# Optimization experiments

Hardware: AMD Instinct MI355X
Metric: run time of the kernel (lower is better)

Reference implementation:

```python
import jax, jax.numpy as jnp
import numpy as np

TAU = 1.0


def setup_inputs() -> dict:
    key = jax.random.key(0)
    k1, k2 = jax.random.split(key)
    z = jax.random.normal(k1, (131072, 64), dtype=jnp.float32)
    cluster_centers = jax.random.normal(k2, (512, 64), dtype=jnp.float32)
    return {"z": z, "cluster_centers": cluster_centers}


def reference(z, cluster_centers):
    # ||z - c||^2 = ||z||^2 + ||c||^2 - 2 z.c  (avoids the [B,K,D] broadcast tensor)
    z_sq = jnp.sum(z * z, axis=1, keepdims=True)              # [B, 1]
    c_sq = jnp.sum(cluster_centers * cluster_centers, axis=1)  # [K]
    cross = jnp.einsum('bd,kd->bk', z, cluster_centers)        # [B, K]
    dist_sq = z_sq + c_sq[None, :] - 2.0 * cross               # [B, K]
    q = jax.nn.softmax(-dist_sq / TAU, axis=1)                 # [B, K]
    loss = jnp.mean(jnp.sum(q * dist_sq, axis=1))
    return (q, loss)
```

## Files before the change

kernel.cpp:

```cpp
#include <hip/hip_runtime.h>

typedef short bf16x8 __attribute__((ext_vector_type(8)));
typedef float f32x4 __attribute__((ext_vector_type(4)));

#define K_CLUSTERS 512
#define DIM 64
#define ROWS_PER_BLOCK 64

__device__ __forceinline__ unsigned short f32_to_bf16_rne(float f) {
    unsigned int u = __float_as_uint(f);
    u += 0x7fffu + ((u >> 16) & 1u);
    return (unsigned short)(u >> 16);
}
__device__ __forceinline__ float bf16_bits_to_f32(unsigned short h) {
    return __uint_as_float(((unsigned int)h) << 16);
}

__global__ void prep_centers(const float* __restrict__ c,
                             short* __restrict__ c_hi, short* __restrict__ c_lo,
                             float* __restrict__ c_sq) {
    int idx = blockIdx.x * 256 + threadIdx.x;
    float v = c[idx];
    unsigned short h = f32_to_bf16_rne(v);
    float hf = bf16_bits_to_f32(h);
    unsigned short l = f32_to_bf16_rne(v - hf);
    c_hi[idx] = (short)h;
    c_lo[idx] = (short)l;
    float s = v * v;
    #pragma unroll
    for (int off = 1; off < 64; off <<= 1) s += __shfl_xor(s, off, 64);
    if ((threadIdx.x & 63) == 0) c_sq[idx >> 6] = s;
}

__global__ void init_loss(float* __restrict__ loss_out) {
    if (threadIdx.x == 0) loss_out[0] = 0.0f;
}

__global__ __launch_bounds__(256, 2)
void cluster_kernel(const float* __restrict__ z,
                    const short* __restrict__ c_hi,
                    const short* __restrict__ c_lo,
                    const float* __restrict__ c_sq,
                    float* __restrict__ q_out,
                    float* __restrict__ loss_out,
                    float inv_b) {
    __shared__ __align__(16) short a_hi_s[16][72];
    __shared__ __align__(16) short a_lo_s[16][72];
    __shared__ float zsq_s[16];
    __shared__ float dist_s[16][K_CLUSTERS + 4];
    __shared__ float wloss_s[4];

    const int tid  = threadIdx.x;
    const int lane = tid & 63;
    const int wave = tid >> 6;
    const int m    = lane & 15;
    const int qd   = lane >> 4;
    const long rb  = (long)blockIdx.x * ROWS_PER_BLOCK;

    bf16x8 bh[8][2], bl[8][2];
    float csq[8];
    #pragma unroll
    for (int t = 0; t < 8; ++t) {
        const int col = wave * 128 + t * 16 + m;
        const long boff = (long)col * DIM + qd * 8;
        #pragma unroll
        for (int kg = 0; kg < 2; ++kg) {
            bh[t][kg] = *(const bf16x8*)(c_hi + boff + kg * 32);
            bl[t][kg] = *(const bf16x8*)(c_lo + boff + kg * 32);
        }
        csq[t] = c_sq[col];
    }

    float4 v = ((const float4*)(z + rb * DIM))[tid];
    float lsum = 0.0f;

    for (int s = 0; s < ROWS_PER_BLOCK / 16; ++s) {
        float4 vn;
        if (s + 1 < ROWS_PER_BLOCK / 16)
            vn = ((const float4*)(z + (rb + (s + 1) * 16) * DIM))[tid];

        {
            const int srow = tid >> 4;
            const int scol = (tid & 15) * 4;
            float fv[4] = {v.x, v.y, v.z, v.w};
            #pragma unroll
            for (int j = 0; j < 4; ++j) {
                unsigned short h = f32_to_bf16_rne(fv[j]);
                float hf = bf16_bits_to_f32(h);
                unsigned short l = f32_to_bf16_rne(fv[j] - hf);
                a_hi_s[srow][scol + j] = (short)h;
                a_lo_s[srow][scol + j] = (short)l;
            }
            float ssq = fv[0]*fv[0] + fv[1]*fv[1] + fv[2]*fv[2] + fv[3]*fv[3];
            #pragma unroll
            for (int off = 1; off < 16; off <<= 1) ssq += __shfl_xor(ssq, off, 64);
            if ((tid & 15) == 0) zsq_s[srow] = ssq;
        }
        __syncthreads();

        bf16x8 ah[2], al[2];
        #pragma unroll
        for (int kg = 0; kg < 2; ++kg) {
            ah[kg] = *(const bf16x8*)&a_hi_s[m][kg * 32 + qd * 8];
            al[kg] = *(const bf16x8*)&a_lo_s[m][kg * 32 + qd * 8];
        }

        f32x4 acc[8];
        #pragma unroll
        for (int t = 0; t < 8; ++t) acc[t] = (f32x4){0.f, 0.f, 0.f, 0.f};
        #pragma unroll
        for (int kg = 0; kg < 2; ++kg) {
            #pragma unroll
            for (int t = 0; t < 8; ++t) {
                acc[t] = __builtin_amdgcn_mfma_f32_16x16x32_bf16(ah[kg], bh[t][kg], acc[t], 0, 0, 0);
                acc[t] = __builtin_amdgcn_mfma_f32_16x16x32_bf16(ah[kg], bl[t][kg], acc[t], 0, 0, 0);
                acc[t] = __builtin_amdgcn_mfma_f32_16x16x32_bf16(al[kg], bh[t][kg], acc[t], 0, 0, 0);
            }
        }

        #pragma unroll
        for (int t = 0; t < 8; ++t) {
            const int col = wave * 128 + t * 16 + m;
            #pragma unroll
            for (int r = 0; r < 4; ++r) {
                const int row = qd * 4 + r;
                dist_s[row][col] = zsq_s[row] + csq[t] - 2.0f * acc[t][r];
            }
        }
        __syncthreads();

        const long rbase = rb + s * 16;
        #pragma unroll
        for (int rr = 0; rr < 4; ++rr) {
            const int row = wave * 4 + rr;
            float d[8];
            #pragma unroll
            for (int j = 0; j < 8; ++j) d[j] = dist_s[row][lane + 64 * j];
            float mn = d[0];
            #pragma unroll
            for (int j = 1; j < 8; ++j) mn = fminf(mn, d[j]);
            #pragma unroll
            for (int off = 1; off < 64; off <<= 1) mn = fminf(mn, __shfl_xor(mn, off, 64));
            float e[8], ssum = 0.0f;
            #pragma unroll
            for (int j = 0; j < 8; ++j) { e[j] = __expf(mn - d[j]); ssum += e[j]; }
            #pragma unroll
            for (int off = 1; off < 64; off <<= 1) ssum += __shfl_xor(ssum, off, 64);
            const float inv = 1.0f / ssum;
            float rl = 0.0f;
            float* orow = q_out + (rbase + row) * K_CLUSTERS;
            #pragma unroll
            for (int j = 0; j < 8; ++j) {
                const float qv = e[j] * inv;
                orow[lane + 64 * j] = qv;
                rl += qv * d[j];
            }
            #pragma unroll
            for (int off = 1; off < 64; off <<= 1) rl += __shfl_xor(rl, off, 64);
            lsum += rl;
        }
        v = vn;
    }

    if (lane == 0) wloss_s[wave] = lsum;
    __syncthreads();
    if (tid == 0)
        atomicAdd(loss_out, (wloss_s[0] + wloss_s[1] + wloss_s[2] + wloss_s[3]) * inv_b);
}

extern "C" void kernel_launch(void* const* d_in, const int* in_sizes, int n_in,
                              void* d_out, int out_size, void* d_ws, size_t ws_size,
                              hipStream_t stream) {
    const float* z = (const float*)d_in[0];
    const float* c = (const float*)d_in[1];
    const int B = in_sizes[0] / DIM;
    float* q_out = (float*)d_out;
    float* loss_out = q_out + (size_t)B * K_CLUSTERS;

    char* ws = (char*)d_ws;
    short* c_hi = (short*)ws;
    short* c_lo = (short*)(ws + 65536);
    float* c_sq = (float*)(ws + 131072);

    prep_centers<<<(K_CLUSTERS * DIM) / 256, 256, 0, stream>>>(c, c_hi, c_lo, c_sq);
    init_loss<<<1, 64, 0, stream>>>(loss_out);
    cluster_kernel<<<B / ROWS_PER_BLOCK, 256, 0, stream>>>(z, c_hi, c_lo, c_sq, q_out,
                                                           loss_out, 1.0f / (float)B);
}
```

Baseline: 343.1 us.

## Split work across 8 waves per block and use nontemporal q stores

Doubles the block to 512 threads so each wave holds centroid fragments for 64 clusters instead of 128 and handles 2 softmax rows instead of 4. This cuts register pressure and raises occupancy. It also writes q with nontemporal stores, moves the loss shuffle reduction out of the row loop, and folds the loss zeroing into prep_centers to drop one launch. The cost is more redundant z staging per block and more barrier participants.

```diff
diff --git a/kernel.cpp b/kernel.cpp
--- a/kernel.cpp
+++ b/kernel.cpp
@@ -18,7 +18,8 @@
 
 __global__ void prep_centers(const float* __restrict__ c,
                              short* __restrict__ c_hi, short* __restrict__ c_lo,
-                             float* __restrict__ c_sq) {
+                             float* __restrict__ c_sq, float* __restrict__ loss_out) {
+    if (blockIdx.x == 0 && threadIdx.x == 0) loss_out[0] = 0.0f;
     int idx = blockIdx.x * 256 + threadIdx.x;
     float v = c[idx];
     unsigned short h = f32_to_bf16_rne(v);
@@ -32,11 +33,7 @@
     if ((threadIdx.x & 63) == 0) c_sq[idx >> 6] = s;
 }
 
-__global__ void init_loss(float* __restrict__ loss_out) {
-    if (threadIdx.x == 0) loss_out[0] = 0.0f;
-}
-
-__global__ __launch_bounds__(256, 2)
+__global__ __launch_bounds__(512, 4)
 void cluster_kernel(const float* __restrict__ z,
                     const short* __restrict__ c_hi,
                     const short* __restrict__ c_lo,
@@ -48,7 +45,7 @@
     __shared__ __align__(16) short a_lo_s[16][72];
     __shared__ float zsq_s[16];
     __shared__ float dist_s[16][K_CLUSTERS + 4];
-    __shared__ float wloss_s[4];
+    __shared__ float wloss_s[8];
 
     const int tid  = threadIdx.x;
     const int lane = tid & 63;
@@ -57,11 +54,11 @@
     const int qd   = lane >> 4;
     const long rb  = (long)blockIdx.x * ROWS_PER_BLOCK;
 
-    bf16x8 bh[8][2], bl[8][2];
-    float csq[8];
+    bf16x8 bh[4][2], bl[4][2];
+    float csq[4];
     #pragma unroll
-    for (int t = 0; t < 8; ++t) {
-        const int col = wave * 128 + t * 16 + m;
+    for (int t = 0; t < 4; ++t) {
+        const int col = wave * 64 + t * 16 + m;
         const long boff = (long)col * DIM + qd * 8;
         #pragma unroll
         for (int kg = 0; kg < 2; ++kg) {
@@ -71,30 +68,30 @@
         csq[t] = c_sq[col];
     }
 
-    float4 v = ((const float4*)(z + rb * DIM))[tid];
+    const float2* zin = (const float2*)(z + rb * DIM);
+    float2 v = zin[tid];
     float lsum = 0.0f;
 
     for (int s = 0; s < ROWS_PER_BLOCK / 16; ++s) {
-        float4 vn;
-        if (s + 1 < ROWS_PER_BLOCK / 16)
-            vn = ((const float4*)(z + (rb + (s + 1) * 16) * DIM))[tid];
+        float2 vn;
+        if (s + 1 < ROWS_PER_BLOCK / 16) vn = zin[(s + 1) * 512 + tid];
 
         {
-            const int srow = tid >> 4;
-            const int scol = (tid & 15) * 4;
-            float fv[4] = {v.x, v.y, v.z, v.w};
+            const int srow = tid >> 5;
+            const int scol = (tid & 31) * 2;
+            float fv[2] = {v.x, v.y};
             #pragma unroll
-            for (int j = 0; j < 4; ++j) {
+            for (int j = 0; j < 2; ++j) {
                 unsigned short h = f32_to_bf16_rne(fv[j]);
                 float hf = bf16_bits_to_f32(h);
                 unsigned short l = f32_to_bf16_rne(fv[j] - hf);
                 a_hi_s[srow][scol + j] = (short)h;
                 a_lo_s[srow][scol + j] = (short)l;
             }
-            float ssq = fv[0]*fv[0] + fv[1]*fv[1] + fv[2]*fv[2] + fv[3]*fv[3];
+            float ssq = fv[0] * fv[0] + fv[1] * fv[1];
             #pragma unroll
-            for (int off = 1; off < 16; off <<= 1) ssq += __shfl_xor(ssq, off, 64);
-            if ((tid & 15) == 0) zsq_s[srow] = ssq;
+            for (int off = 1; off < 32; off <<= 1) ssq += __shfl_xor(ssq, off, 64);
+            if ((tid & 31) == 0) zsq_s[srow] = ssq;
         }
         __syncthreads();
 
@@ -105,13 +102,13 @@
             al[kg] = *(const bf16x8*)&a_lo_s[m][kg * 32 + qd * 8];
         }
 
-        f32x4 acc[8];
+        f32x4 acc[4];
         #pragma unroll
-        for (int t = 0; t < 8; ++t) acc[t] = (f32x4){0.f, 0.f, 0.f, 0.f};
+        for (int t = 0; t < 4; ++t) acc[t] = (f32x4){0.f, 0.f, 0.f, 0.f};
         #pragma unroll
         for (int kg = 0; kg < 2; ++kg) {
             #pragma unroll
-            for (int t = 0; t < 8; ++t) {
+            for (int t = 0; t < 4; ++t) {
                 acc[t] = __builtin_amdgcn_mfma_f32_16x16x32_bf16(ah[kg], bh[t][kg], acc[t], 0, 0, 0);
                 acc[t] = __builtin_amdgcn_mfma_f32_16x16x32_bf16(ah[kg], bl[t][kg], acc[t], 0, 0, 0);
                 acc[t] = __builtin_amdgcn_mfma_f32_16x16x32_bf16(al[kg], bh[t][kg], acc[t], 0, 0, 0);
@@ -119,8 +116,8 @@
         }
 
         #pragma unroll
-        for (int t = 0; t < 8; ++t) {
-            const int col = wave * 128 + t * 16 + m;
+        for (int t = 0; t < 4; ++t) {
+            const int col = wave * 64 + t * 16 + m;
             #pragma unroll
             for (int r = 0; r < 4; ++r) {
                 const int row = qd * 4 + r;
@@ -131,8 +128,8 @@
 
         const long rbase = rb + s * 16;
         #pragma unroll
-        for (int rr = 0; rr < 4; ++rr) {
-            const int row = wave * 4 + rr;
+        for (int rr = 0; rr < 2; ++rr) {
+            const int row = wave * 2 + rr;
             float d[8];
             #pragma unroll
             for (int j = 0; j < 8; ++j) d[j] = dist_s[row][lane + 64 * j];
@@ -152,20 +149,24 @@
             #pragma unroll
             for (int j = 0; j < 8; ++j) {
                 const float qv = e[j] * inv;
-                orow[lane + 64 * j] = qv;
+                __builtin_nontemporal_store(qv, orow + lane + 64 * j);
                 rl += qv * d[j];
             }
-            #pragma unroll
-            for (int off = 1; off < 64; off <<= 1) rl += __shfl_xor(rl, off, 64);
             lsum += rl;
         }
         v = vn;
     }
 
+    #pragma unroll
+    for (int off = 1; off < 64; off <<= 1) lsum += __shfl_xor(lsum, off, 64);
     if (lane == 0) wloss_s[wave] = lsum;
     __syncthreads();
-    if (tid == 0)
-        atomicAdd(loss_out, (wloss_s[0] + wloss_s[1] + wloss_s[2] + wloss_s[3]) * inv_b);
+    if (tid == 0) {
+        float t0 = 0.f;
+        #pragma unroll
+        for (int w = 0; w < 8; ++w) t0 += wloss_s[w];
+        atomicAdd(loss_out, t0 * inv_b);
+    }
 }
 
 extern "C" void kernel_launch(void* const* d_in, const int* in_sizes, int n_in,
@@ -182,8 +183,7 @@
     short* c_lo = (short*)(ws + 65536);
     float* c_sq = (float*)(ws + 131072);
 
-    prep_centers<<<(K_CLUSTERS * DIM) / 256, 256, 0, stream>>>(c, c_hi, c_lo, c_sq);
-    init_loss<<<1, 64, 0, stream>>>(loss_out);
-    cluster_kernel<<<B / ROWS_PER_BLOCK, 256, 0, stream>>>(z, c_hi, c_lo, c_sq, q_out,
+    prep_centers<<<(K_CLUSTERS * DIM) / 256, 256, 0, stream>>>(c, c_hi, c_lo, c_sq, loss_out);
+    cluster_kernel<<<B / ROWS_PER_BLOCK, 512, 0, stream>>>(z, c_hi, c_lo, c_sq, q_out,
                                                            loss_out, 1.0f / (float)B);
 }
```

New measurement: 342.2 us. Within noise of the previous version (-0.3%).
